# Kernel tuning notes

Measured on AMD Instinct MI355X. Metric: run time of the kernel, lower is better.

## Reference

```python
import jax, jax.numpy as jnp
import numpy as np

N_NODES = 100000
N_EDGES = 1600000
F_IN = 64
HID = 32
HEADS = 4
NEG_SLOPE = 0.2  # PyG GATConv default
EPS = 1e-16      # PyG softmax denominator epsilon


def gat_layer(x, edge_index, W, a_src, a_dst, bias, heads, out_ch, concat):
    """PyG-style GATConv (eval mode: dropout disabled), add_self_loops=True.
    x: [N, F]; edge_index: [2, E] (row0=source j, row1=target i);
    W: [F, heads*out_ch]; a_src/a_dst: [heads, out_ch]; bias: [heads*out_ch] or [out_ch].
    """
    N = x.shape[0]
    loops = jnp.arange(N)
    src = jnp.concatenate([edge_index[0], loops])  # [E+N]
    dst = jnp.concatenate([edge_index[1], loops])
    h = (x @ W).reshape(N, heads, out_ch)           # [N, H, C]
    alpha_s = jnp.einsum('nhc,hc->nh', h, a_src)    # [N, H]
    alpha_d = jnp.einsum('nhc,hc->nh', h, a_dst)
    e = jax.nn.leaky_relu(alpha_s[src] + alpha_d[dst], NEG_SLOPE)  # [E+N, H]
    # numerically stable scatter-softmax over incoming edges per target node
    m = jax.ops.segment_max(e, dst, num_segments=N)                # [N, H]
    ex = jnp.exp(e - m[dst])
    denom = jax.ops.segment_sum(ex, dst, num_segments=N)           # [N, H]
    alpha = ex / (denom[dst] + EPS)                                # [E+N, H]
    msg = h[src] * alpha[..., None]                                # [E+N, H, C]
    out = jax.ops.segment_sum(msg, dst, num_segments=N)            # [N, H, C]
    out = out.reshape(N, heads * out_ch) if concat else out.mean(axis=1)
    return out + bias


def setup_inputs() -> dict:
    key = jax.random.key(0)
    ks = jax.random.split(key, 12)
    glorot = lambda k, shape: jax.random.normal(k, shape, jnp.float32) * np.sqrt(2.0 / (shape[0] + shape[-1]))
    x = jax.random.normal(ks[0], (N_NODES, F_IN), jnp.float32)
    edge_index = jax.random.randint(ks[1], (2, N_EDGES), 0, N_NODES, jnp.int64 if jax.config.jax_enable_x64 else jnp.int32)
    batch = jnp.zeros((N_NODES,), jnp.int32)
    return {
        'x': x,
        'edge_index': edge_index,
        'batch': batch,
        'W1': glorot(ks[2], (F_IN, HEADS * HID)),
        'a_src1': glorot(ks[3], (HEADS, HID)),
        'a_dst1': glorot(ks[4], (HEADS, HID)),
        'b1': jnp.zeros((HEADS * HID,), jnp.float32),
        'W2': glorot(ks[5], (HEADS * HID, HID)),
        'a_src2': glorot(ks[6], (1, HID)),
        'a_dst2': glorot(ks[7], (1, HID)),
        'b2': jnp.zeros((HID,), jnp.float32),
        'W_lin': glorot(ks[8], (HID, 1)),
        'b_lin': jnp.zeros((1,), jnp.float32),
    }


def reference(x, edge_index, batch, W1, a_src1, a_dst1, b1, W2, a_src2, a_dst2, b2, W_lin, b_lin):
    h = jax.nn.relu(gat_layer(x, edge_index, W1, a_src1, a_dst1, b1, HEADS, HID, concat=True))
    h = jax.nn.relu(gat_layer(h, edge_index, W2, a_src2, a_dst2, b2, 1, HID, concat=False))
    out = h @ W_lin + b_lin  # [N, 1]
    return out.squeeze(-1)
```

## Files before the change

### kernel.cpp

```cpp
#include <hip/hip_runtime.h>
#include <math.h>

#define NEG_SLOPE 0.2f
#define EPS 1e-16f

__device__ inline float leaky(float v) {
    return v >= 0.0f ? v : NEG_SLOPE * v;
}

__device__ inline unsigned bf16pack2(float a, float b) {
    unsigned ua = __float_as_uint(a);
    unsigned ub = __float_as_uint(b);
    ua = (ua + 0x7FFFu + ((ua >> 16) & 1u)) >> 16;
    ub = (ub + 0x7FFFu + ((ub >> 16) & 1u)) >> 16;
    return ua | (ub << 16);
}

__device__ inline float bf16lo(unsigned u) { return __uint_as_float(u << 16); }
__device__ inline float bf16hi(unsigned u) { return __uint_as_float(u & 0xFFFF0000u); }

__global__ __launch_bounds__(256) void k_init(int* deg, int N) {
    int gid = blockIdx.x * blockDim.x + threadIdx.x;
    if (gid < N) deg[gid] = 1;
}

__global__ __launch_bounds__(256) void k_hist(const int* __restrict__ ei, int* __restrict__ deg, int E) {
    int e = blockIdx.x * blockDim.x + threadIdx.x;
    if (e < E) atomicAdd(&deg[ei[E + e]], 1);
}

__global__ __launch_bounds__(256) void k_scan1(const int* __restrict__ deg, int* __restrict__ rowptr,
                                               int* __restrict__ blocksum, int N) {
    __shared__ int s[256];
    int tid = threadIdx.x;
    int i = blockIdx.x * 256 + tid;
    int v = (i < N) ? deg[i] : 0;
    s[tid] = v;
    __syncthreads();
#pragma unroll
    for (int off = 1; off < 256; off <<= 1) {
        int t = (tid >= off) ? s[tid - off] : 0;
        __syncthreads();
        s[tid] += t;
        __syncthreads();
    }
    if (i < N) rowptr[i] = s[tid] - v;
    if (tid == 255) blocksum[blockIdx.x] = s[255];
}

__global__ __launch_bounds__(512) void k_scan2(int* __restrict__ blocksum, int nb) {
    __shared__ int s[512];
    int tid = threadIdx.x;
    int v = (tid < nb) ? blocksum[tid] : 0;
    s[tid] = v;
    __syncthreads();
#pragma unroll
    for (int off = 1; off < 512; off <<= 1) {
        int t = (tid >= off) ? s[tid - off] : 0;
        __syncthreads();
        s[tid] += t;
        __syncthreads();
    }
    if (tid < nb) blocksum[tid] = s[tid] - v;
}

__global__ __launch_bounds__(256) void k_scan3(int* __restrict__ rowptr, const int* __restrict__ blocksum,
                                               int* __restrict__ cursor, int N, int total) {
    int i = blockIdx.x * blockDim.x + threadIdx.x;
    if (i < N) {
        int v = rowptr[i] + blocksum[i >> 8];
        rowptr[i] = v;
        cursor[i] = v;
    }
    if (i == 0) rowptr[N] = total;
}

__global__ __launch_bounds__(256) void k_fill(const int* __restrict__ ei,
                                              int* __restrict__ cursor, int* __restrict__ col,
                                              int E, int N) {
    int e = blockIdx.x * blockDim.x + threadIdx.x;
    if (e >= E + N) return;
    int src, dst;
    if (e < E) { src = ei[e]; dst = ei[E + e]; }
    else       { src = dst = e - E; }
    int pos = atomicAdd(&cursor[dst], 1);
    col[pos] = src;
}

__global__ __launch_bounds__(256) void k_gemm1(const float* __restrict__ x,
                                               const float* __restrict__ W1,
                                               const float* __restrict__ a_src,
                                               const float* __restrict__ a_dst,
                                               unsigned* __restrict__ h1bf,
                                               float* __restrict__ as1,
                                               float* __restrict__ ad1, int N) {
    __shared__ float sW[64 * 128];
    __shared__ float sX[32 * 64];
    int tid = threadIdx.x;
    int block_r0 = blockIdx.x * 32;

    {
        float4* dst = (float4*)sW;
        const float4* srcp = (const float4*)W1;
#pragma unroll
        for (int i = 0; i < 8; ++i) dst[tid + 256 * i] = srcp[tid + 256 * i];
    }
    {
        float4* dst = (float4*)sX;
#pragma unroll
        for (int i = 0; i < 2; ++i) {
            int idx = tid + 256 * i;
            int r = idx >> 4;
            int c = idx & 15;
            int gr = min(block_r0 + r, N - 1);
            dst[idx] = ((const float4*)(x + (size_t)gr * 64))[c];
        }
    }
    __syncthreads();

    int c4 = tid & 31;
    int rq = tid >> 5;
    int r0 = block_r0 + rq * 4;
    const float4* wS = (const float4*)sW;
    const float4* xS = (const float4*)sX;

    float4 acc0 = {0,0,0,0}, acc1 = {0,0,0,0}, acc2 = {0,0,0,0}, acc3 = {0,0,0,0};
#pragma unroll 2
    for (int k4 = 0; k4 < 16; ++k4) {
        float4 xa = xS[(rq * 4 + 0) * 16 + k4];
        float4 xb = xS[(rq * 4 + 1) * 16 + k4];
        float4 xc = xS[(rq * 4 + 2) * 16 + k4];
        float4 xd = xS[(rq * 4 + 3) * 16 + k4];
        float4 w0 = wS[(k4 * 4 + 0) * 32 + c4];
        float4 w1 = wS[(k4 * 4 + 1) * 32 + c4];
        float4 w2 = wS[(k4 * 4 + 2) * 32 + c4];
        float4 w3 = wS[(k4 * 4 + 3) * 32 + c4];
        acc0.x += xa.x*w0.x + xa.y*w1.x + xa.z*w2.x + xa.w*w3.x;
        acc0.y += xa.x*w0.y + xa.y*w1.y + xa.z*w2.y + xa.w*w3.y;
        acc0.z += xa.x*w0.z + xa.y*w1.z + xa.z*w2.z + xa.w*w3.z;
        acc0.w += xa.x*w0.w + xa.y*w1.w + xa.z*w2.w + xa.w*w3.w;
        acc1.x += xb.x*w0.x + xb.y*w1.x + xb.z*w2.x + xb.w*w3.x;
        acc1.y += xb.x*w0.y + xb.y*w1.y + xb.z*w2.y + xb.w*w3.y;
        acc1.z += xb.x*w0.z + xb.y*w1.z + xb.z*w2.z + xb.w*w3.z;
        acc1.w += xb.x*w0.w + xb.y*w1.w + xb.z*w2.w + xb.w*w3.w;
        acc2.x += xc.x*w0.x + xc.y*w1.x + xc.z*w2.x + xc.w*w3.x;
        acc2.y += xc.x*w0.y + xc.y*w1.y + xc.z*w2.y + xc.w*w3.y;
        acc2.z += xc.x*w0.z + xc.y*w1.z + xc.z*w2.z + xc.w*w3.z;
        acc2.w += xc.x*w0.w + xc.y*w1.w + xc.z*w2.w + xc.w*w3.w;
        acc3.x += xd.x*w0.x + xd.y*w1.x + xd.z*w2.x + xd.w*w3.x;
        acc3.y += xd.x*w0.y + xd.y*w1.y + xd.z*w2.y + xd.w*w3.y;
        acc3.z += xd.x*w0.z + xd.y*w1.z + xd.z*w2.z + xd.w*w3.z;
        acc3.w += xd.x*w0.w + xd.y*w1.w + xd.z*w2.w + xd.w*w3.w;
    }

    uint2 p0 = { bf16pack2(acc0.x, acc0.y), bf16pack2(acc0.z, acc0.w) };
    uint2 p1 = { bf16pack2(acc1.x, acc1.y), bf16pack2(acc1.z, acc1.w) };
    uint2 p2 = { bf16pack2(acc2.x, acc2.y), bf16pack2(acc2.z, acc2.w) };
    uint2 p3 = { bf16pack2(acc3.x, acc3.y), bf16pack2(acc3.z, acc3.w) };
    uint2* hb = (uint2*)h1bf;
    if (r0 + 0 < N) hb[(size_t)(r0 + 0) * 32 + c4] = p0;
    if (r0 + 1 < N) hb[(size_t)(r0 + 1) * 32 + c4] = p1;
    if (r0 + 2 < N) hb[(size_t)(r0 + 2) * 32 + c4] = p2;
    if (r0 + 3 < N) hb[(size_t)(r0 + 3) * 32 + c4] = p3;

    float4 av = ((const float4*)a_src)[c4];
    float4 dv = ((const float4*)a_dst)[c4];
    float s0 = acc0.x*av.x + acc0.y*av.y + acc0.z*av.z + acc0.w*av.w;
    float s1 = acc1.x*av.x + acc1.y*av.y + acc1.z*av.z + acc1.w*av.w;
    float s2 = acc2.x*av.x + acc2.y*av.y + acc2.z*av.z + acc2.w*av.w;
    float s3 = acc3.x*av.x + acc3.y*av.y + acc3.z*av.z + acc3.w*av.w;
    float d0 = acc0.x*dv.x + acc0.y*dv.y + acc0.z*dv.z + acc0.w*dv.w;
    float d1 = acc1.x*dv.x + acc1.y*dv.y + acc1.z*dv.z + acc1.w*dv.w;
    float d2 = acc2.x*dv.x + acc2.y*dv.y + acc2.z*dv.z + acc2.w*dv.w;
    float d3 = acc3.x*dv.x + acc3.y*dv.y + acc3.z*dv.z + acc3.w*dv.w;
#pragma unroll
    for (int off = 1; off < 8; off <<= 1) {
        s0 += __shfl_xor(s0, off); s1 += __shfl_xor(s1, off);
        s2 += __shfl_xor(s2, off); s3 += __shfl_xor(s3, off);
        d0 += __shfl_xor(d0, off); d1 += __shfl_xor(d1, off);
        d2 += __shfl_xor(d2, off); d3 += __shfl_xor(d3, off);
    }
    if ((c4 & 7) == 0) {
        int h = c4 >> 3;
        if (r0 + 0 < N) { as1[(r0 + 0) * 4 + h] = s0; ad1[(r0 + 0) * 4 + h] = d0; }
        if (r0 + 1 < N) { as1[(r0 + 1) * 4 + h] = s1; ad1[(r0 + 1) * 4 + h] = d1; }
        if (r0 + 2 < N) { as1[(r0 + 2) * 4 + h] = s2; ad1[(r0 + 2) * 4 + h] = d2; }
        if (r0 + 3 < N) { as1[(r0 + 3) * 4 + h] = s3; ad1[(r0 + 3) * 4 + h] = d3; }
    }
}

__global__ __launch_bounds__(256) void k_gather1(const int* __restrict__ rowptr,
                                                 const int* __restrict__ col,
                                                 const float* __restrict__ as1,
                                                 const float* __restrict__ ad1,
                                                 const unsigned* __restrict__ h1bf,
                                                 const float* __restrict__ b1,
                                                 float* __restrict__ out1, int N) {
    int tid = threadIdx.x;
    int wid = (blockIdx.x * blockDim.x + tid) >> 6;
    if (wid >= N) return;
    int lane = tid & 63;
    int dst = wid;
    int start = rowptr[dst], end = rowptr[dst + 1];
    float4 ad = *(const float4*)(ad1 + (size_t)dst * 4);

    float m0 = -INFINITY, m1 = -INFINITY, m2 = -INFINITY, m3 = -INFINITY;
    for (int j = start + lane; j < end; j += 64) {
        int src = col[j];
        float4 a = *(const float4*)(as1 + (size_t)src * 4);
        m0 = fmaxf(m0, leaky(a.x + ad.x));
        m1 = fmaxf(m1, leaky(a.y + ad.y));
        m2 = fmaxf(m2, leaky(a.z + ad.z));
        m3 = fmaxf(m3, leaky(a.w + ad.w));
    }
#pragma unroll
    for (int off = 32; off; off >>= 1) {
        m0 = fmaxf(m0, __shfl_xor(m0, off));
        m1 = fmaxf(m1, __shfl_xor(m1, off));
        m2 = fmaxf(m2, __shfl_xor(m2, off));
        m3 = fmaxf(m3, __shfl_xor(m3, off));
    }

    int h = lane >> 4;
    float mh  = (h == 0) ? m0 : (h == 1) ? m1 : (h == 2) ? m2 : m3;
    float adh = (h == 0) ? ad.x : (h == 1) ? ad.y : (h == 2) ? ad.z : ad.w;

    float acc0 = 0.0f, acc1 = 0.0f, den = 0.0f;
    int j = start;
    for (; j + 3 < end; j += 4) {
        int s0 = col[j], s1 = col[j + 1], s2 = col[j + 2], s3 = col[j + 3];
        float a0 = as1[s0 * 4 + h];
        float a1 = as1[s1 * 4 + h];
        float a2 = as1[s2 * 4 + h];
        float a3 = as1[s3 * 4 + h];
        unsigned u0 = h1bf[(size_t)s0 * 64 + lane];
        unsigned u1 = h1bf[(size_t)s1 * 64 + lane];
        unsigned u2 = h1bf[(size_t)s2 * 64 + lane];
        unsigned u3 = h1bf[(size_t)s3 * 64 + lane];
        float x0 = __expf(leaky(a0 + adh) - mh);
        float x1 = __expf(leaky(a1 + adh) - mh);
        float x2 = __expf(leaky(a2 + adh) - mh);
        float x3 = __expf(leaky(a3 + adh) - mh);
        den += (x0 + x1) + (x2 + x3);
        acc0 += x0 * bf16lo(u0) + x1 * bf16lo(u1) + x2 * bf16lo(u2) + x3 * bf16lo(u3);
        acc1 += x0 * bf16hi(u0) + x1 * bf16hi(u1) + x2 * bf16hi(u2) + x3 * bf16hi(u3);
    }
    for (; j < end; ++j) {
        int src = col[j];
        float ex = __expf(leaky(as1[src * 4 + h] + adh) - mh);
        unsigned u = h1bf[(size_t)src * 64 + lane];
        den += ex;
        acc0 += ex * bf16lo(u);
        acc1 += ex * bf16hi(u);
    }

    float inv = 1.0f / (den + EPS);
    int f0 = 2 * lane;
    float vA = acc0 * inv + b1[f0];
    float vB = acc1 * inv + b1[f0 + 1];
    float2 o;
    o.x = vA > 0.0f ? vA : 0.0f;
    o.y = vB > 0.0f ? vB : 0.0f;
    *(float2*)(out1 + (size_t)dst * 128 + f0) = o;
}

__global__ __launch_bounds__(256) void k_gemm2(const float* __restrict__ out1,
                                               const float* __restrict__ W2,
                                               const float* __restrict__ a_src,
                                               const float* __restrict__ a_dst,
                                               unsigned* __restrict__ h2bf,
                                               float* __restrict__ as2,
                                               float* __restrict__ ad2, int N) {
    __shared__ float sW[128 * 32];
    int tid = threadIdx.x;

    {
        float4* dst = (float4*)sW;
        const float4* srcp = (const float4*)W2;
#pragma unroll
        for (int i = 0; i < 4; ++i) dst[tid + 256 * i] = srcp[tid + 256 * i];
    }
    __syncthreads();

    int c4 = tid & 7;
    int rq = tid >> 3;
    int r0 = blockIdx.x * 128 + rq * 4;
    if (r0 >= N) return;
    const float* xr0 = out1 + (size_t)min(r0 + 0, N - 1) * 128;
    const float* xr1 = out1 + (size_t)min(r0 + 1, N - 1) * 128;
    const float* xr2 = out1 + (size_t)min(r0 + 2, N - 1) * 128;
    const float* xr3 = out1 + (size_t)min(r0 + 3, N - 1) * 128;
    const float4* wS = (const float4*)sW;

    float4 acc0 = {0,0,0,0}, acc1 = {0,0,0,0}, acc2 = {0,0,0,0}, acc3 = {0,0,0,0};
#pragma unroll 2
    for (int k4 = 0; k4 < 32; ++k4) {
        float4 xa = *(const float4*)(xr0 + k4 * 4);
        float4 xb = *(const float4*)(xr1 + k4 * 4);
        float4 xc = *(const float4*)(xr2 + k4 * 4);
        float4 xd = *(const float4*)(xr3 + k4 * 4);
        float4 w0 = wS[(k4 * 4 + 0) * 8 + c4];
        float4 w1 = wS[(k4 * 4 + 1) * 8 + c4];
        float4 w2 = wS[(k4 * 4 + 2) * 8 + c4];
        float4 w3 = wS[(k4 * 4 + 3) * 8 + c4];
        acc0.x += xa.x*w0.x + xa.y*w1.x + xa.z*w2.x + xa.w*w3.x;
        acc0.y += xa.x*w0.y + xa.y*w1.y + xa.z*w2.y + xa.w*w3.y;
        acc0.z += xa.x*w0.z + xa.y*w1.z + xa.z*w2.z + xa.w*w3.z;
        acc0.w += xa.x*w0.w + xa.y*w1.w + xa.z*w2.w + xa.w*w3.w;
        acc1.x += xb.x*w0.x + xb.y*w1.x + xb.z*w2.x + xb.w*w3.x;
        acc1.y += xb.x*w0.y + xb.y*w1.y + xb.z*w2.y + xb.w*w3.y;
        acc1.z += xb.x*w0.z + xb.y*w1.z + xb.z*w2.z + xb.w*w3.z;
        acc1.w += xb.x*w0.w + xb.y*w1.w + xb.z*w2.w + xb.w*w3.w;
        acc2.x += xc.x*w0.x + xc.y*w1.x + xc.z*w2.x + xc.w*w3.x;
        acc2.y += xc.x*w0.y + xc.y*w1.y + xc.z*w2.y + xc.w*w3.y;
        acc2.z += xc.x*w0.z + xc.y*w1.z + xc.z*w2.z + xc.w*w3.z;
        acc2.w += xc.x*w0.w + xc.y*w1.w + xc.z*w2.w + xc.w*w3.w;
        acc3.x += xd.x*w0.x + xd.y*w1.x + xd.z*w2.x + xd.w*w3.x;
        acc3.y += xd.x*w0.y + xd.y*w1.y + xd.z*w2.y + xd.w*w3.y;
        acc3.z += xd.x*w0.z + xd.y*w1.z + xd.z*w2.z + xd.w*w3.z;
        acc3.w += xd.x*w0.w + xd.y*w1.w + xd.z*w2.w + xd.w*w3.w;
    }

    uint2 q0 = { bf16pack2(acc0.x, acc0.y), bf16pack2(acc0.z, acc0.w) };
    uint2 q1 = { bf16pack2(acc1.x, acc1.y), bf16pack2(acc1.z, acc1.w) };
    uint2 q2 = { bf16pack2(acc2.x, acc2.y), bf16pack2(acc2.z, acc2.w) };
    uint2 q3 = { bf16pack2(acc3.x, acc3.y), bf16pack2(acc3.z, acc3.w) };
    uint2* hb = (uint2*)h2bf;
    if (r0 + 0 < N) hb[(size_t)(r0 + 0) * 8 + c4] = q0;
    if (r0 + 1 < N) hb[(size_t)(r0 + 1) * 8 + c4] = q1;
    if (r0 + 2 < N) hb[(size_t)(r0 + 2) * 8 + c4] = q2;
    if (r0 + 3 < N) hb[(size_t)(r0 + 3) * 8 + c4] = q3;

    float4 av = ((const float4*)a_src)[c4];
    float4 dv = ((const float4*)a_dst)[c4];
    float s0 = acc0.x*av.x + acc0.y*av.y + acc0.z*av.z + acc0.w*av.w;
    float s1 = acc1.x*av.x + acc1.y*av.y + acc1.z*av.z + acc1.w*av.w;
    float s2 = acc2.x*av.x + acc2.y*av.y + acc2.z*av.z + acc2.w*av.w;
    float s3 = acc3.x*av.x + acc3.y*av.y + acc3.z*av.z + acc3.w*av.w;
    float d0 = acc0.x*dv.x + acc0.y*dv.y + acc0.z*dv.z + acc0.w*dv.w;
    float d1 = acc1.x*dv.x + acc1.y*dv.y + acc1.z*dv.z + acc1.w*dv.w;
    float d2 = acc2.x*dv.x + acc2.y*dv.y + acc2.z*dv.z + acc2.w*dv.w;
    float d3 = acc3.x*dv.x + acc3.y*dv.y + acc3.z*dv.z + acc3.w*dv.w;
#pragma unroll
    for (int off = 1; off < 8; off <<= 1) {
        s0 += __shfl_xor(s0, off); s1 += __shfl_xor(s1, off);
        s2 += __shfl_xor(s2, off); s3 += __shfl_xor(s3, off);
        d0 += __shfl_xor(d0, off); d1 += __shfl_xor(d1, off);
        d2 += __shfl_xor(d2, off); d3 += __shfl_xor(d3, off);
    }
    if (c4 == 0) {
        if (r0 + 0 < N) { as2[r0 + 0] = s0; ad2[r0 + 0] = d0; }
        if (r0 + 1 < N) { as2[r0 + 1] = s1; ad2[r0 + 1] = d1; }
        if (r0 + 2 < N) { as2[r0 + 2] = s2; ad2[r0 + 2] = d2; }
        if (r0 + 3 < N) { as2[r0 + 3] = s3; ad2[r0 + 3] = d3; }
    }
}

__global__ __launch_bounds__(256) void k_gather2(const int* __restrict__ rowptr,
                                                 const int* __restrict__ col,
                                                 const float* __restrict__ as2,
                                                 const float* __restrict__ ad2,
                                                 const unsigned short* __restrict__ h2b,
                                                 const float* __restrict__ b2,
                                                 const float* __restrict__ W_lin,
                                                 const float* __restrict__ b_lin,
                                                 float* __restrict__ out, int N) {
    int tid = threadIdx.x;
    int swid = (blockIdx.x * blockDim.x + tid) >> 5;
    if (swid >= N) return;
    int c = tid & 31;
    int dst = swid;
    int start = rowptr[dst], end = rowptr[dst + 1];
    float adv = ad2[dst];

    float m = -INFINITY;
    for (int j = start + c; j < end; j += 32) {
        m = fmaxf(m, leaky(as2[col[j]] + adv));
    }
#pragma unroll
    for (int off = 16; off; off >>= 1) m = fmaxf(m, __shfl_xor(m, off, 32));

    float acc = 0.0f, den = 0.0f;
    int j = start;
    for (; j + 3 < end; j += 4) {
        int s0 = col[j], s1 = col[j + 1], s2 = col[j + 2], s3 = col[j + 3];
        float a0 = as2[s0], a1 = as2[s1], a2 = as2[s2], a3 = as2[s3];
        unsigned short u0 = h2b[(size_t)s0 * 32 + c];
        unsigned short u1 = h2b[(size_t)s1 * 32 + c];
        unsigned short u2 = h2b[(size_t)s2 * 32 + c];
        unsigned short u3 = h2b[(size_t)s3 * 32 + c];
        float x0 = __expf(leaky(a0 + adv) - m);
        float x1 = __expf(leaky(a1 + adv) - m);
        float x2 = __expf(leaky(a2 + adv) - m);
        float x3 = __expf(leaky(a3 + adv) - m);
        den += (x0 + x1) + (x2 + x3);
        acc += x0 * __uint_as_float(((unsigned)u0) << 16)
             + x1 * __uint_as_float(((unsigned)u1) << 16)
             + x2 * __uint_as_float(((unsigned)u2) << 16)
             + x3 * __uint_as_float(((unsigned)u3) << 16);
    }
    for (; j < end; ++j) {
        int src = col[j];
        float ex = __expf(leaky(as2[src] + adv) - m);
        unsigned short u = h2b[(size_t)src * 32 + c];
        den += ex;
        acc += ex * __uint_as_float(((unsigned)u) << 16);
    }

    float v = acc / (den + EPS) + b2[c];
    v = v > 0.0f ? v : 0.0f;

    float w = v * W_lin[c];
#pragma unroll
    for (int off = 16; off; off >>= 1) w += __shfl_xor(w, off, 32);
    if (c == 0) out[dst] = w + b_lin[0];
}

extern "C" void kernel_launch(void* const* d_in, const int* in_sizes, int n_in,
                              void* d_out, int out_size, void* d_ws, size_t ws_size,
                              hipStream_t stream) {
    const float* x      = (const float*)d_in[0];
    const int*   ei     = (const int*)d_in[1];
    const float* W1     = (const float*)d_in[3];
    const float* a_src1 = (const float*)d_in[4];
    const float* a_dst1 = (const float*)d_in[5];
    const float* b1     = (const float*)d_in[6];
    const float* W2     = (const float*)d_in[7];
    const float* a_src2 = (const float*)d_in[8];
    const float* a_dst2 = (const float*)d_in[9];
    const float* b2     = (const float*)d_in[10];
    const float* W_lin  = (const float*)d_in[11];
    const float* b_lin  = (const float*)d_in[12];
    float* out = (float*)d_out;

    const int N = in_sizes[0] / 64;
    const int E = in_sizes[1] / 2;
    const int T = E + N;
    const int NB = (N + 255) / 256;

    float* ws = (float*)d_ws;
    size_t off = 0;
    float* h1reg = ws + off; off += (size_t)N * 128;
    float* out1 = ws + off; off += (size_t)N * 128;
    float* as1  = ws + off; off += (size_t)N * 4;
    float* ad1  = ws + off; off += (size_t)N * 4;
    float* as2  = ws + off; off += (size_t)N;
    float* ad2  = ws + off; off += (size_t)N;
    int* deg      = (int*)(ws + off); off += (size_t)N;
    int* cursor   = (int*)(ws + off); off += (size_t)N;
    int* rowptr   = (int*)(ws + off); off += (size_t)N + 4;
    int* blocksum = (int*)(ws + off); off += 1024;
    int* colarr   = (int*)(ws + off); off += (size_t)T;
    unsigned* h1bf = (unsigned*)h1reg;
    unsigned* h2bf = (unsigned*)h1reg;

    const int B = 256;
    auto blocks = [](size_t t, int b) { return (unsigned)((t + b - 1) / b); };

    k_init <<<blocks(N, B), B, 0, stream>>>(deg, N);
    k_hist <<<blocks(E, B), B, 0, stream>>>(ei, deg, E);
    k_scan1<<<NB, 256, 0, stream>>>(deg, rowptr, blocksum, N);
    k_scan2<<<1, 512, 0, stream>>>(blocksum, NB);
    k_scan3<<<blocks(N, B), B, 0, stream>>>(rowptr, blocksum, cursor, N, T);
    k_fill <<<blocks(T, B), B, 0, stream>>>(ei, cursor, colarr, E, N);

    k_gemm1  <<<(unsigned)((N + 31) / 32), B, 0, stream>>>(x, W1, a_src1, a_dst1, h1bf, as1, ad1, N);
    k_gather1<<<blocks((size_t)N * 64, B), B, 0, stream>>>(rowptr, colarr, as1, ad1, h1bf, b1, out1, N);

    k_gemm2  <<<(unsigned)((N + 127) / 128), B, 0, stream>>>(out1, W2, a_src2, a_dst2, h2bf, as2, ad2, N);
    k_gather2<<<blocks((size_t)N * 32, B), B, 0, stream>>>(rowptr, colarr, as2, ad2,
                                                           (const unsigned short*)h2bf, b2, W_lin, b_lin, out, N);
}
```

Measured before the change: 490.5 us.

## Bucket edges by destination block before CSR fill to localize atomics

Self-loop column entries are now written directly during the scan, so the fill pass handles only real edges. The CSR fill becomes a two-pass bucket sort. Edges are first scattered into per-128-node buckets using a small set of counters, then a second pass does the per-destination atomic placement from the bucketed pairs. This gives better locality for the cursor atomics and col writes, in exchange for an extra kernel launch and an extra write and read of the pair buffer. The pair buffer reuses the out1 workspace.

```diff
diff --git a/kernel.cpp b/kernel.cpp
--- a/kernel.cpp
+++ b/kernel.cpp
@@ -65,26 +65,43 @@
 }
 
 __global__ __launch_bounds__(256) void k_scan3(int* __restrict__ rowptr, const int* __restrict__ blocksum,
-                                               int* __restrict__ cursor, int N, int total) {
+                                               int* __restrict__ cursor, int* __restrict__ col,
+                                               int N, int total) {
     int i = blockIdx.x * blockDim.x + threadIdx.x;
     if (i < N) {
         int v = rowptr[i] + blocksum[i >> 8];
         rowptr[i] = v;
-        cursor[i] = v;
+        cursor[i] = v + 1;
+        col[v] = i;
     }
     if (i == 0) rowptr[N] = total;
 }
 
-__global__ __launch_bounds__(256) void k_fill(const int* __restrict__ ei,
-                                              int* __restrict__ cursor, int* __restrict__ col,
-                                              int E, int N) {
+__global__ __launch_bounds__(256) void k_bseed(const int* __restrict__ rowptr, int* __restrict__ bcur,
+                                               int N, int NBK) {
+    int b = blockIdx.x * blockDim.x + threadIdx.x;
+    if (b < NBK) {
+        int node = min(b << 7, N);
+        bcur[b] = rowptr[node] - node;
+    }
+}
+
+__global__ __launch_bounds__(256) void k_bscat(const int* __restrict__ ei, int* __restrict__ bcur,
+                                               int2* __restrict__ pairs, int E) {
     int e = blockIdx.x * blockDim.x + threadIdx.x;
-    if (e >= E + N) return;
-    int src, dst;
-    if (e < E) { src = ei[e]; dst = ei[E + e]; }
-    else       { src = dst = e - E; }
-    int pos = atomicAdd(&cursor[dst], 1);
-    col[pos] = src;
+    if (e >= E) return;
+    int s = ei[e], d = ei[E + e];
+    int p = atomicAdd(&bcur[d >> 7], 1);
+    pairs[p] = make_int2(s, d);
+}
+
+__global__ __launch_bounds__(256) void k_fill2(const int2* __restrict__ pairs,
+                                               int* __restrict__ cursor, int* __restrict__ col, int E) {
+    int e = blockIdx.x * blockDim.x + threadIdx.x;
+    if (e >= E) return;
+    int2 pr = pairs[e];
+    int pos = atomicAdd(&cursor[pr.y], 1);
+    col[pos] = pr.x;
 }
 
 __global__ __launch_bounds__(256) void k_gemm1(const float* __restrict__ x,
@@ -437,6 +454,7 @@
     const int E = in_sizes[1] / 2;
     const int T = E + N;
     const int NB = (N + 255) / 256;
+    const int NBK = (N + 127) >> 7;
 
     float* ws = (float*)d_ws;
     size_t off = 0;
@@ -451,8 +469,10 @@
     int* rowptr   = (int*)(ws + off); off += (size_t)N + 4;
     int* blocksum = (int*)(ws + off); off += 1024;
     int* colarr   = (int*)(ws + off); off += (size_t)T;
+    int* bcur     = (int*)(ws + off); off += (size_t)NBK + 4;
     unsigned* h1bf = (unsigned*)h1reg;
     unsigned* h2bf = (unsigned*)h1reg;
+    int2* pairs = (int2*)out1;
 
     const int B = 256;
     auto blocks = [](size_t t, int b) { return (unsigned)((t + b - 1) / b); };
@@ -461,8 +481,10 @@
     k_hist <<<blocks(E, B), B, 0, stream>>>(ei, deg, E);
     k_scan1<<<NB, 256, 0, stream>>>(deg, rowptr, blocksum, N);
     k_scan2<<<1, 512, 0, stream>>>(blocksum, NB);
-    k_scan3<<<blocks(N, B), B, 0, stream>>>(rowptr, blocksum, cursor, N, T);
-    k_fill <<<blocks(T, B), B, 0, stream>>>(ei, cursor, colarr, E, N);
+    k_scan3<<<blocks(N, B), B, 0, stream>>>(rowptr, blocksum, cursor, colarr, N, T);
+    k_bseed<<<blocks(NBK, B), B, 0, stream>>>(rowptr, bcur, N, NBK);
+    k_bscat<<<blocks(E, B), B, 0, stream>>>(ei, bcur, pairs, E);
+    k_fill2<<<blocks(E, B), B, 0, stream>>>(pairs, cursor, colarr, E);
 
     k_gemm1  <<<(unsigned)((N + 31) / 32), B, 0, stream>>>(x, W1, a_src1, a_dst1, h1bf, as1, ad1, N);
     k_gather1<<<blocks((size_t)N * 64, B), B, 0, stream>>>(rowptr, colarr, as1, ad1, h1bf, b1, out1, N);
```

After: 790.3 us. +61.1%, slower.
